# Performance work log

Measured on AMD Instinct MI355X. Metric: run time of the kernel, lower is better.

Reference implementation:

```python
import jax, jax.numpy as jnp
import numpy as np

PAD = -10000.0
B, N, F = 512, 2048, 16
H_PHI, LAT, H_RHO = 128, 128, 128


def _xavier(key, fan_in, fan_out):
    bound = np.sqrt(6.0 / (fan_in + fan_out))
    return jax.random.uniform(key, (fan_in, fan_out), jnp.float32, -bound, bound)


def setup_inputs() -> dict:
    key = jax.random.key(0)
    ks = jax.random.split(key, 12)
    x = jax.random.normal(ks[0], (B, N, F), jnp.float32)
    # ragged set lengths: pad tail rows with -10000.0 (the module's padding sentinel)
    lengths = jax.random.randint(ks[1], (B,), 1, N + 1)
    pad_mask = jnp.arange(N)[None, :] >= lengths[:, None]  # True where padded
    x = jnp.where(pad_mask[:, :, None], PAD, x)
    params = {
        "phi_w0": _xavier(ks[2], F, H_PHI), "phi_b0": jnp.zeros((H_PHI,), jnp.float32),
        "phi_w1": _xavier(ks[3], H_PHI, H_PHI), "phi_b1": jnp.zeros((H_PHI,), jnp.float32),
        "phi_w2": _xavier(ks[4], H_PHI, H_PHI), "phi_b2": jnp.zeros((H_PHI,), jnp.float32),
        "phi_w3": _xavier(ks[5], H_PHI, LAT), "phi_b3": jnp.zeros((LAT,), jnp.float32),
        "rho_w0": _xavier(ks[6], LAT, H_RHO), "rho_b0": jnp.zeros((H_RHO,), jnp.float32),
        "rho_w1": _xavier(ks[7], H_RHO, H_RHO), "rho_b1": jnp.zeros((H_RHO,), jnp.float32),
        "rho_w2": _xavier(ks[8], H_RHO, H_RHO), "rho_b2": jnp.zeros((H_RHO,), jnp.float32),
        "rho_w3": _xavier(ks[9], H_RHO, 1), "rho_b3": jnp.zeros((1,), jnp.float32),
    }
    return {"inputs": x, **params}


def reference(inputs, phi_w0, phi_b0, phi_w1, phi_b1, phi_w2, phi_b2, phi_w3, phi_b3,
              rho_w0, rho_b0, rho_w1, rho_b1, rho_w2, rho_b2, rho_w3, rho_b3):
    b, n, f = inputs.shape
    # valid-prefix mask: sum rows before the FIRST all-(-10000) row (matches torch loop)
    is_pad = jnp.all(inputs == PAD, axis=-1)                       # [B,N]
    first = jnp.where(jnp.any(is_pad, axis=-1), jnp.argmax(is_pad, axis=-1), n)
    mask = (jnp.arange(n)[None, :] < first[:, None]).astype(inputs.dtype)  # [B,N]
    relu = jax.nn.relu
    # phi applied per point
    h = relu(inputs @ phi_w0 + phi_b0)
    h = relu(h @ phi_w1 + phi_b1)
    h = relu(h @ phi_w2 + phi_b2)
    h = relu(h @ phi_w3 + phi_b3)                                  # [B,N,LAT]
    # masked variable-length sum pooling (segment reduce)
    pooled = jnp.einsum('bnd,bn->bd', h, mask)                     # [B,LAT]
    r = relu(pooled @ rho_w0 + rho_b0)
    r = relu(r @ rho_w1 + rho_b1)
    r = relu(r @ rho_w2 + rho_b2)
    cost = (r @ rho_w3 + rho_b3)[:, 0]                             # [B]
    return cost
```

## Files before the change

kernel.cpp:

```cpp
#include <hip/hip_runtime.h>

typedef _Float16 f16;
typedef f16  f16x2  __attribute__((ext_vector_type(2)));
typedef f16  f16x8  __attribute__((ext_vector_type(8)));
typedef __fp16 h16x2 __attribute__((ext_vector_type(2)));
typedef float f32x16 __attribute__((ext_vector_type(16)));

#define B_   512
#define N_   2048
#define PADV -10000.0f

union F16x8 { f16x8 v; f16x2 h2[4]; };

__device__ __forceinline__ f16x2 pkrtz(float a, float b) {
    h16x2 r = __builtin_amdgcn_cvt_pkrtz(a, b);
    return __builtin_bit_cast(f16x2, r);
}

__global__ void prep_kernel(const float* __restrict__ w0, const float* __restrict__ w1,
                            const float* __restrict__ w2, const float* __restrict__ w3,
                            f16* __restrict__ out, float* __restrict__ pooled)
{
    int i = blockIdx.x * 256 + threadIdx.x;
    if (i < 2048) {
        out[i] = (f16)w0[(i & 15) * 128 + (i >> 4)];
    } else if (i < 51200) {
        int j = i - 2048;
        int l = j >> 14, r = j & 16383;
        int o = r >> 7, slot = r & 127;
        int s = slot >> 4, qq = (slot >> 3) & 1, jj = slot & 7;
        int sig = 32 * (s >> 1) + 16 * (s & 1) + 4 * qq + 8 * (jj >> 2) + (jj & 3);
        const float* w = (l == 0) ? w1 : (l == 1) ? w2 : w3;
        out[i] = (f16)w[sig * 128 + o];
    }
    pooled[i] = 0.f;
}

__device__ __forceinline__ int swz(int row, int chunk) {
    return row * 256 + ((chunk ^ (row & 15)) << 4);
}

__device__ __forceinline__ void gl_lds16(const void* g, void* l) {
    __builtin_amdgcn_global_load_lds(
        (const __attribute__((address_space(1))) void*)g,
        (__attribute__((address_space(3))) void*)l, 16, 0, 0);
}

__global__ __launch_bounds__(256, 2) void phi_pool_kernel(
    const float* __restrict__ x,
    const f16*  __restrict__ wtbuf,
    const float* __restrict__ pb0, const float* __restrict__ pb1,
    const float* __restrict__ pb2, const float* __restrict__ pb3,
    float* __restrict__ pooled)
{
    __shared__ f16 wA[16384];
    __shared__ f16 wB[16384];

    const int tid  = threadIdx.x;
    const int lane = tid & 63;
    const int wv   = tid >> 6;
    const int l31  = lane & 31;
    const int q    = lane >> 5;
    const int b    = blockIdx.x & 511;
    const int tile0 = (blockIdx.x >> 9) * 256;

    {
        const float4 f0 = *(const float4*)(x + ((size_t)b * N_ + tile0) * 16);
        if (f0.x == PADV && f0.y == PADV && f0.z == PADV && f0.w == PADV) return;
    }

    const int p0 = tile0 + wv * 64;

    const float* xp = x + ((size_t)b * N_ + (size_t)(p0 + l31)) * 16 + 8 * q;
    float4 a0 = ((const float4*)xp)[0];
    float4 a1 = ((const float4*)xp)[1];
    float4 c0 = ((const float4*)(xp + 512))[0];
    float4 c1 = ((const float4*)(xp + 512))[1];

    f16x8 w0f[4];
    #pragma unroll
    for (int c = 0; c < 4; ++c)
        w0f[c] = *(const f16x8*)(wtbuf + (32 * c + l31) * 16 + 8 * q);

    {
        const f16* wl1 = wtbuf + 2048;
        const f16* wl2 = wtbuf + 2048 + 16384;
        #pragma unroll
        for (int i = 0; i < 8; ++i) {
            const int row   = wv * 32 + i * 4 + (lane >> 4);
            const int chunk = (lane & 15) ^ (row & 15);
            const int loff  = (wv * 32 + i * 4) * 256;
            gl_lds16(wl1 + row * 128 + chunk * 8, (char*)wA + loff);
            gl_lds16(wl2 + row * 128 + chunk * 8, (char*)wB + loff);
        }
    }

    bool vA = (a0.x != PADV) || (a0.y != PADV) || (a0.z != PADV) || (a0.w != PADV) ||
              (a1.x != PADV) || (a1.y != PADV) || (a1.z != PADV) || (a1.w != PADV);
    bool vB = (c0.x != PADV) || (c0.y != PADV) || (c0.z != PADV) || (c0.w != PADV) ||
              (c1.x != PADV) || (c1.y != PADV) || (c1.z != PADV) || (c1.w != PADV);
    unsigned long long blA = __ballot(vA), blB = __ballot(vB);
    const unsigned mA = (unsigned)blA | (unsigned)(blA >> 32);
    const unsigned mB = (unsigned)blB | (unsigned)(blB >> 32);

    F16x8 hf[2][8];
    hf[0][0].h2[0] = pkrtz(a0.x, a0.y);
    hf[0][0].h2[1] = pkrtz(a0.z, a0.w);
    hf[0][0].h2[2] = pkrtz(a1.x, a1.y);
    hf[0][0].h2[3] = pkrtz(a1.z, a1.w);
    hf[1][0].h2[0] = pkrtz(c0.x, c0.y);
    hf[1][0].h2[1] = pkrtz(c0.z, c0.w);
    hf[1][0].h2[2] = pkrtz(c1.x, c1.y);
    hf[1][0].h2[3] = pkrtz(c1.z, c1.w);

    f32x16 acc[2][4];

    #define INIT_ACC_BIAS(pb)                                              \
        {                                                                  \
            _Pragma("unroll")                                              \
            for (int c = 0; c < 4; ++c) {                                  \
                _Pragma("unroll")                                          \
                for (int g = 0; g < 4; ++g) {                              \
                    float4 bb = *(const float4*)((pb) + 32 * c + 8 * g + 4 * q); \
                    const float* bbp = (const float*)&bb;                  \
                    _Pragma("unroll")                                      \
                    for (int e = 0; e < 4; ++e) {                          \
                        acc[0][c][4 * g + e] = bbp[e];                     \
                        acc[1][c][4 * g + e] = bbp[e];                     \
                    }                                                      \
                }                                                          \
            }                                                              \
        }

    #define EPILOGUE()                                                     \
        {                                                                  \
            const f16x2 z2 = {(f16)0.f, (f16)0.f};                         \
            _Pragma("unroll")                                              \
            for (int t = 0; t < 2; ++t) {                                  \
                _Pragma("unroll")                                          \
                for (int s = 0; s < 8; ++s) {                              \
                    const int c = s >> 1, r0 = 8 * (s & 1);                \
                    _Pragma("unroll")                                      \
                    for (int p = 0; p < 4; ++p) {                          \
                        f16x2 m = pkrtz(                                   \
                            acc[t][c][r0 + 2 * p], acc[t][c][r0 + 2 * p + 1]); \
                        hf[t][s].h2[p] = __builtin_elementwise_max(m, z2); \
                    }                                                      \
                }                                                          \
            }                                                              \
        }

    INIT_ACC_BIAS(pb0);
    #pragma unroll
    for (int c = 0; c < 4; ++c) {
        acc[0][c] = __builtin_amdgcn_mfma_f32_32x32x16_f16(w0f[c], hf[0][0].v, acc[0][c], 0, 0, 0);
        acc[1][c] = __builtin_amdgcn_mfma_f32_32x32x16_f16(w0f[c], hf[1][0].v, acc[1][c], 0, 0, 0);
    }
    EPILOGUE();

    __syncthreads();

    INIT_ACC_BIAS(pb1);
    #pragma unroll
    for (int s = 0; s < 8; ++s) {
        f16x8 wf[4];
        #pragma unroll
        for (int c = 0; c < 4; ++c)
            wf[c] = *(const f16x8*)((const char*)wA + swz(32 * c + l31, 2 * s + q));
        #pragma unroll
        for (int c = 0; c < 4; ++c) {
            acc[0][c] = __builtin_amdgcn_mfma_f32_32x32x16_f16(wf[c], hf[0][s].v, acc[0][c], 0, 0, 0);
            acc[1][c] = __builtin_amdgcn_mfma_f32_32x32x16_f16(wf[c], hf[1][s].v, acc[1][c], 0, 0, 0);
        }
    }

    __syncthreads();

    {
        const f16* wl3 = wtbuf + 2048 + 32768;
        #pragma unroll
        for (int i = 0; i < 8; ++i) {
            const int row   = wv * 32 + i * 4 + (lane >> 4);
            const int chunk = (lane & 15) ^ (row & 15);
            const int loff  = (wv * 32 + i * 4) * 256;
            gl_lds16(wl3 + row * 128 + chunk * 8, (char*)wA + loff);
        }
    }

    EPILOGUE();

    INIT_ACC_BIAS(pb2);
    #pragma unroll
    for (int s = 0; s < 8; ++s) {
        f16x8 wf[4];
        #pragma unroll
        for (int c = 0; c < 4; ++c)
            wf[c] = *(const f16x8*)((const char*)wB + swz(32 * c + l31, 2 * s + q));
        #pragma unroll
        for (int c = 0; c < 4; ++c) {
            acc[0][c] = __builtin_amdgcn_mfma_f32_32x32x16_f16(wf[c], hf[0][s].v, acc[0][c], 0, 0, 0);
            acc[1][c] = __builtin_amdgcn_mfma_f32_32x32x16_f16(wf[c], hf[1][s].v, acc[1][c], 0, 0, 0);
        }
    }
    EPILOGUE();

    __syncthreads();

    {
        float bL[4];
        #pragma unroll
        for (int c = 0; c < 4; ++c) bL[c] = pb3[32 * c + l31];
        #pragma unroll
        for (int t = 0; t < 2; ++t)
            #pragma unroll
            for (int c = 0; c < 4; ++c)
                #pragma unroll
                for (int r = 0; r < 16; ++r) acc[t][c][r] = bL[c];
    }
    #pragma unroll
    for (int s = 0; s < 8; ++s) {
        f16x8 wf[4];
        #pragma unroll
        for (int c = 0; c < 4; ++c)
            wf[c] = *(const f16x8*)((const char*)wA + swz(32 * c + l31, 2 * s + q));
        #pragma unroll
        for (int c = 0; c < 4; ++c) {
            acc[0][c] = __builtin_amdgcn_mfma_f32_32x32x16_f16(hf[0][s].v, wf[c], acc[0][c], 0, 0, 0);
            acc[1][c] = __builtin_amdgcn_mfma_f32_32x32x16_f16(hf[1][s].v, wf[c], acc[1][c], 0, 0, 0);
        }
    }

    #pragma unroll
    for (int c = 0; c < 4; ++c) {
        float s0 = 0.f;
        #pragma unroll
        for (int t = 0; t < 2; ++t) {
            const unsigned m = t ? mB : mA;
            #pragma unroll
            for (int r = 0; r < 16; ++r) {
                const int ptl = 4 * q + (r & 3) + 8 * (r >> 2);
                float v = fmaxf(acc[t][c][r], 0.f);
                s0 += ((m >> ptl) & 1u) ? v : 0.f;
            }
        }
        s0 += __shfl_xor(s0, 32);
        if (q == 0) atomicAdd(&pooled[b * 128 + 32 * c + l31], s0);
    }
}

__global__ __launch_bounds__(128) void rho_kernel(
    const float* __restrict__ pooled,
    const float* __restrict__ w0, const float* __restrict__ b0,
    const float* __restrict__ w1, const float* __restrict__ b1,
    const float* __restrict__ w2, const float* __restrict__ b2,
    const float* __restrict__ w3, const float* __restrict__ b3,
    float* __restrict__ out)
{
    __shared__ float buf[2][128];
    __shared__ float red[2];
    const int b = blockIdx.x, t = threadIdx.x;
    buf[0][t] = pooled[b * 128 + t];
    __syncthreads();
    const float* ws3[3] = {w0, w1, w2};
    const float* bs3[3] = {b0, b1, b2};
    int cur = 0;
    #pragma unroll 1
    for (int l = 0; l < 3; ++l) {
        float acc = bs3[l][t];
        const float* w = ws3[l];
        #pragma unroll 8
        for (int k = 0; k < 128; ++k)
            acc = fmaf(buf[cur][k], w[k * 128 + t], acc);
        buf[cur ^ 1][t] = fmaxf(acc, 0.f);
        cur ^= 1;
        __syncthreads();
    }
    float v = buf[cur][t] * w3[t];
    #pragma unroll
    for (int off = 32; off > 0; off >>= 1)
        v += __shfl_down(v, off, 64);
    if ((t & 63) == 0) red[t >> 6] = v;
    __syncthreads();
    if (t == 0) out[b] = red[0] + red[1] + b3[0];
}

extern "C" void kernel_launch(void* const* d_in, const int* in_sizes, int n_in,
                              void* d_out, int out_size, void* d_ws, size_t ws_size,
                              hipStream_t stream)
{
    (void)in_sizes; (void)n_in; (void)out_size; (void)ws_size;
    const float* x      = (const float*)d_in[0];
    const float* phi_w0 = (const float*)d_in[1];
    const float* phi_b0 = (const float*)d_in[2];
    const float* phi_w1 = (const float*)d_in[3];
    const float* phi_b1 = (const float*)d_in[4];
    const float* phi_w2 = (const float*)d_in[5];
    const float* phi_b2 = (const float*)d_in[6];
    const float* phi_w3 = (const float*)d_in[7];
    const float* phi_b3 = (const float*)d_in[8];
    const float* rho_w0 = (const float*)d_in[9];
    const float* rho_b0 = (const float*)d_in[10];
    const float* rho_w1 = (const float*)d_in[11];
    const float* rho_b1 = (const float*)d_in[12];
    const float* rho_w2 = (const float*)d_in[13];
    const float* rho_b2 = (const float*)d_in[14];
    const float* rho_w3 = (const float*)d_in[15];
    const float* rho_b3 = (const float*)d_in[16];

    float* pooled = (float*)d_ws;
    f16*   wtbuf  = (f16*)((char*)d_ws + 262144);

    prep_kernel<<<256, 256, 0, stream>>>(phi_w0, phi_w1, phi_w2, phi_w3, wtbuf, pooled);
    phi_pool_kernel<<<4096, 256, 0, stream>>>(x, wtbuf, phi_b0, phi_b1, phi_b2, phi_b3, pooled);
    rho_kernel<<<B_, 128, 0, stream>>>(pooled, rho_w0, rho_b0, rho_w1, rho_b1,
                                       rho_w2, rho_b2, rho_w3, rho_b3, (float*)d_out);
}
```

Measured before the change: 205.0 us.

## Halve per-block tile and use single LDS weight buffer for higher occupancy

Each block now handles 128 points instead of 256, with one 32-point MFMA tile per wave instead of two. The grid doubles to 8192 blocks and launch bounds rise to 4 blocks per CU. The two 32KB LDS weight buffers become one 32KB buffer that is restaged for each layer, with extra barriers between layers. This is meant to raise occupancy and give finer early exit on padded tiles. The cost is less reuse of the weights pulled from LDS, and weight staging becomes serialized behind the barriers.

```diff
diff --git a/kernel.cpp b/kernel.cpp
--- a/kernel.cpp
+++ b/kernel.cpp
@@ -46,15 +46,14 @@
         (__attribute__((address_space(3))) void*)l, 16, 0, 0);
 }
 
-__global__ __launch_bounds__(256, 2) void phi_pool_kernel(
+__global__ __launch_bounds__(256, 4) void phi_pool_kernel(
     const float* __restrict__ x,
     const f16*  __restrict__ wtbuf,
     const float* __restrict__ pb0, const float* __restrict__ pb1,
     const float* __restrict__ pb2, const float* __restrict__ pb3,
     float* __restrict__ pooled)
 {
-    __shared__ f16 wA[16384];
-    __shared__ f16 wB[16384];
+    __shared__ f16 wS[16384];
 
     const int tid  = threadIdx.x;
     const int lane = tid & 63;
@@ -62,58 +61,49 @@
     const int l31  = lane & 31;
     const int q    = lane >> 5;
     const int b    = blockIdx.x & 511;
-    const int tile0 = (blockIdx.x >> 9) * 256;
+    const int tile0 = (blockIdx.x >> 9) * 128;
 
     {
         const float4 f0 = *(const float4*)(x + ((size_t)b * N_ + tile0) * 16);
         if (f0.x == PADV && f0.y == PADV && f0.z == PADV && f0.w == PADV) return;
     }
 
-    const int p0 = tile0 + wv * 64;
+    const int p0 = tile0 + wv * 32;
 
     const float* xp = x + ((size_t)b * N_ + (size_t)(p0 + l31)) * 16 + 8 * q;
     float4 a0 = ((const float4*)xp)[0];
     float4 a1 = ((const float4*)xp)[1];
-    float4 c0 = ((const float4*)(xp + 512))[0];
-    float4 c1 = ((const float4*)(xp + 512))[1];
 
     f16x8 w0f[4];
     #pragma unroll
     for (int c = 0; c < 4; ++c)
         w0f[c] = *(const f16x8*)(wtbuf + (32 * c + l31) * 16 + 8 * q);
 
-    {
-        const f16* wl1 = wtbuf + 2048;
-        const f16* wl2 = wtbuf + 2048 + 16384;
-        #pragma unroll
-        for (int i = 0; i < 8; ++i) {
-            const int row   = wv * 32 + i * 4 + (lane >> 4);
-            const int chunk = (lane & 15) ^ (row & 15);
-            const int loff  = (wv * 32 + i * 4) * 256;
-            gl_lds16(wl1 + row * 128 + chunk * 8, (char*)wA + loff);
-            gl_lds16(wl2 + row * 128 + chunk * 8, (char*)wB + loff);
-        }
-    }
+#define STAGE(src)                                                      \
+    {                                                                   \
+        _Pragma("unroll")                                               \
+        for (int i = 0; i < 8; ++i) {                                   \
+            const int row   = wv * 32 + i * 4 + (lane >> 4);            \
+            const int chunk = (lane & 15) ^ (row & 15);                 \
+            const int loff  = (wv * 32 + i * 4) * 256;   \
+            gl_lds16((src) + row * 128 + chunk * 8, (char*)wS + loff);  \
+        }                                                               \
+    }
+
+    STAGE(wtbuf + 2048);
 
     bool vA = (a0.x != PADV) || (a0.y != PADV) || (a0.z != PADV) || (a0.w != PADV) ||
               (a1.x != PADV) || (a1.y != PADV) || (a1.z != PADV) || (a1.w != PADV);
-    bool vB = (c0.x != PADV) || (c0.y != PADV) || (c0.z != PADV) || (c0.w != PADV) ||
-              (c1.x != PADV) || (c1.y != PADV) || (c1.z != PADV) || (c1.w != PADV);
-    unsigned long long blA = __ballot(vA), blB = __ballot(vB);
+    unsigned long long blA = __ballot(vA);
     const unsigned mA = (unsigned)blA | (unsigned)(blA >> 32);
-    const unsigned mB = (unsigned)blB | (unsigned)(blB >> 32);
-
-    F16x8 hf[2][8];
-    hf[0][0].h2[0] = pkrtz(a0.x, a0.y);
-    hf[0][0].h2[1] = pkrtz(a0.z, a0.w);
-    hf[0][0].h2[2] = pkrtz(a1.x, a1.y);
-    hf[0][0].h2[3] = pkrtz(a1.z, a1.w);
-    hf[1][0].h2[0] = pkrtz(c0.x, c0.y);
-    hf[1][0].h2[1] = pkrtz(c0.z, c0.w);
-    hf[1][0].h2[2] = pkrtz(c1.x, c1.y);
-    hf[1][0].h2[3] = pkrtz(c1.z, c1.w);
-
-    f32x16 acc[2][4];
+
+    F16x8 hf[8];
+    hf[0].h2[0] = pkrtz(a0.x, a0.y);
+    hf[0].h2[1] = pkrtz(a0.z, a0.w);
+    hf[0].h2[2] = pkrtz(a1.x, a1.y);
+    hf[0].h2[3] = pkrtz(a1.z, a1.w);
+
+    f32x16 acc[4];
 
     #define INIT_ACC_BIAS(pb)                                              \
         {                                                                  \
@@ -124,10 +114,8 @@
                     float4 bb = *(const float4*)((pb) + 32 * c + 8 * g + 4 * q); \
                     const float* bbp = (const float*)&bb;                  \
                     _Pragma("unroll")                                      \
-                    for (int e = 0; e < 4; ++e) {                          \
-                        acc[0][c][4 * g + e] = bbp[e];                     \
-                        acc[1][c][4 * g + e] = bbp[e];                     \
-                    }                                                      \
+                    for (int e = 0; e < 4; ++e)                            \
+                        acc[c][4 * g + e] = bbp[e];                        \
                 }                                                          \
             }                                                              \
         }
@@ -136,112 +124,88 @@
         {                                                                  \
             const f16x2 z2 = {(f16)0.f, (f16)0.f};                         \
             _Pragma("unroll")                                              \
-            for (int t = 0; t < 2; ++t) {                                  \
+            for (int s = 0; s < 8; ++s) {                                  \
+                const int c = s >> 1, r0 = 8 * (s & 1);                    \
                 _Pragma("unroll")                                          \
-                for (int s = 0; s < 8; ++s) {                              \
-                    const int c = s >> 1, r0 = 8 * (s & 1);                \
-                    _Pragma("unroll")                                      \
-                    for (int p = 0; p < 4; ++p) {                          \
-                        f16x2 m = pkrtz(                                   \
-                            acc[t][c][r0 + 2 * p], acc[t][c][r0 + 2 * p + 1]); \
-                        hf[t][s].h2[p] = __builtin_elementwise_max(m, z2); \
-                    }                                                      \
+                for (int p = 0; p < 4; ++p) {                              \
+                    f16x2 m = pkrtz(                                       \
+                        acc[c][r0 + 2 * p], acc[c][r0 + 2 * p + 1]);       \
+                    hf[s].h2[p] = __builtin_elementwise_max(m, z2);        \
                 }                                                          \
             }                                                              \
         }
 
     INIT_ACC_BIAS(pb0);
     #pragma unroll
-    for (int c = 0; c < 4; ++c) {
-        acc[0][c] = __builtin_amdgcn_mfma_f32_32x32x16_f16(w0f[c], hf[0][0].v, acc[0][c], 0, 0, 0);
-        acc[1][c] = __builtin_amdgcn_mfma_f32_32x32x16_f16(w0f[c], hf[1][0].v, acc[1][c], 0, 0, 0);
-    }
+    for (int c = 0; c < 4; ++c)
+        acc[c] = __builtin_amdgcn_mfma_f32_32x32x16_f16(w0f[c], hf[0].v, acc[c], 0, 0, 0);
     EPILOGUE();
-
-    __syncthreads();
-
     INIT_ACC_BIAS(pb1);
+
+    __syncthreads();
+
     #pragma unroll
     for (int s = 0; s < 8; ++s) {
         f16x8 wf[4];
         #pragma unroll
         for (int c = 0; c < 4; ++c)
-            wf[c] = *(const f16x8*)((const char*)wA + swz(32 * c + l31, 2 * s + q));
-        #pragma unroll
-        for (int c = 0; c < 4; ++c) {
-            acc[0][c] = __builtin_amdgcn_mfma_f32_32x32x16_f16(wf[c], hf[0][s].v, acc[0][c], 0, 0, 0);
-            acc[1][c] = __builtin_amdgcn_mfma_f32_32x32x16_f16(wf[c], hf[1][s].v, acc[1][c], 0, 0, 0);
-        }
-    }
-
-    __syncthreads();
-
-    {
-        const f16* wl3 = wtbuf + 2048 + 32768;
-        #pragma unroll
-        for (int i = 0; i < 8; ++i) {
-            const int row   = wv * 32 + i * 4 + (lane >> 4);
-            const int chunk = (lane & 15) ^ (row & 15);
-            const int loff  = (wv * 32 + i * 4) * 256;
-            gl_lds16(wl3 + row * 128 + chunk * 8, (char*)wA + loff);
-        }
-    }
-
+            wf[c] = *(const f16x8*)((const char*)wS + swz(32 * c + l31, 2 * s + q));
+        #pragma unroll
+        for (int c = 0; c < 4; ++c)
+            acc[c] = __builtin_amdgcn_mfma_f32_32x32x16_f16(wf[c], hf[s].v, acc[c], 0, 0, 0);
+    }
+
+    __syncthreads();
+    STAGE(wtbuf + 2048 + 16384);
     EPILOGUE();
-
     INIT_ACC_BIAS(pb2);
+    __syncthreads();
+
     #pragma unroll
     for (int s = 0; s < 8; ++s) {
         f16x8 wf[4];
         #pragma unroll
         for (int c = 0; c < 4; ++c)
-            wf[c] = *(const f16x8*)((const char*)wB + swz(32 * c + l31, 2 * s + q));
-        #pragma unroll
-        for (int c = 0; c < 4; ++c) {
-            acc[0][c] = __builtin_amdgcn_mfma_f32_32x32x16_f16(wf[c], hf[0][s].v, acc[0][c], 0, 0, 0);
-            acc[1][c] = __builtin_amdgcn_mfma_f32_32x32x16_f16(wf[c], hf[1][s].v, acc[1][c], 0, 0, 0);
-        }
-    }
+            wf[c] = *(const f16x8*)((const char*)wS + swz(32 * c + l31, 2 * s + q));
+        #pragma unroll
+        for (int c = 0; c < 4; ++c)
+            acc[c] = __builtin_amdgcn_mfma_f32_32x32x16_f16(wf[c], hf[s].v, acc[c], 0, 0, 0);
+    }
+
+    __syncthreads();
+    STAGE(wtbuf + 2048 + 32768);
     EPILOGUE();
-
-    __syncthreads();
 
     {
         float bL[4];
         #pragma unroll
         for (int c = 0; c < 4; ++c) bL[c] = pb3[32 * c + l31];
         #pragma unroll
-        for (int t = 0; t < 2; ++t)
+        for (int c = 0; c < 4; ++c)
             #pragma unroll
-            for (int c = 0; c < 4; ++c)
-                #pragma unroll
-                for (int r = 0; r < 16; ++r) acc[t][c][r] = bL[c];
-    }
+            for (int r = 0; r < 16; ++r) acc[c][r] = bL[c];
+    }
+    __syncthreads();
+
     #pragma unroll
     for (int s = 0; s < 8; ++s) {
         f16x8 wf[4];
         #pragma unroll
         for (int c = 0; c < 4; ++c)
-            wf[c] = *(const f16x8*)((const char*)wA + swz(32 * c + l31, 2 * s + q));
-        #pragma unroll
-        for (int c = 0; c < 4; ++c) {
-            acc[0][c] = __builtin_amdgcn_mfma_f32_32x32x16_f16(hf[0][s].v, wf[c], acc[0][c], 0, 0, 0);
-            acc[1][c] = __builtin_amdgcn_mfma_f32_32x32x16_f16(hf[1][s].v, wf[c], acc[1][c], 0, 0, 0);
-        }
+            wf[c] = *(const f16x8*)((const char*)wS + swz(32 * c + l31, 2 * s + q));
+        #pragma unroll
+        for (int c = 0; c < 4; ++c)
+            acc[c] = __builtin_amdgcn_mfma_f32_32x32x16_f16(hf[s].v, wf[c], acc[c], 0, 0, 0);
     }
 
     #pragma unroll
     for (int c = 0; c < 4; ++c) {
         float s0 = 0.f;
         #pragma unroll
-        for (int t = 0; t < 2; ++t) {
-            const unsigned m = t ? mB : mA;
-            #pragma unroll
-            for (int r = 0; r < 16; ++r) {
-                const int ptl = 4 * q + (r & 3) + 8 * (r >> 2);
-                float v = fmaxf(acc[t][c][r], 0.f);
-                s0 += ((m >> ptl) & 1u) ? v : 0.f;
-            }
+        for (int r = 0; r < 16; ++r) {
+            const int ptl = 4 * q + (r & 3) + 8 * (r >> 2);
+            float v = fmaxf(acc[c][r], 0.f);
+            s0 += ((mA >> ptl) & 1u) ? v : 0.f;
         }
         s0 += __shfl_xor(s0, 32);
         if (q == 0) atomicAdd(&pooled[b * 128 + 32 * c + l31], s0);
@@ -311,7 +275,7 @@
     f16*   wtbuf  = (f16*)((char*)d_ws + 262144);
 
     prep_kernel<<<256, 256, 0, stream>>>(phi_w0, phi_w1, phi_w2, phi_w3, wtbuf, pooled);
-    phi_pool_kernel<<<4096, 256, 0, stream>>>(x, wtbuf, phi_b0, phi_b1, phi_b2, phi_b3, pooled);
+    phi_pool_kernel<<<8192, 256, 0, stream>>>(x, wtbuf, phi_b0, phi_b1, phi_b2, phi_b3, pooled);
     rho_kernel<<<B_, 128, 0, stream>>>(pooled, rho_w0, rho_b0, rho_w1, rho_b1,
                                        rho_w2, rho_b2, rho_w3, rho_b3, (float*)d_out);
 }
```

Measured after the change: 265.0 us. 1.29x slower.

## Convert phi kernel to persistent blocks with work-stealing and resident layer weights

Applied to the files above, without the earlier changes.

Swaps the 4096-block grid, which reloaded layer weights into LDS for every 256-point tile, for 256 persistent 512-thread blocks. Each block loads all three 128x128 layer weights into 96KB of dynamic LDS once, then its waves pull (tile, batch-group) work items from per-wave atomic counters initialised in the prep kernel. This amortises weight staging and removes the intra-block barriers between layers. In exchange it uses more LDS per block, which lowers occupancy, adds atomic contention on the counters, and handles one 64-point tile per wave iteration rather than a 256-point block.

```diff
diff --git a/kernel.cpp b/kernel.cpp
--- a/kernel.cpp
+++ b/kernel.cpp
@@ -19,7 +19,8 @@
 
 __global__ void prep_kernel(const float* __restrict__ w0, const float* __restrict__ w1,
                             const float* __restrict__ w2, const float* __restrict__ w3,
-                            f16* __restrict__ out, float* __restrict__ pooled)
+                            f16* __restrict__ out, float* __restrict__ pooled,
+                            unsigned* __restrict__ cnt)
 {
     int i = blockIdx.x * 256 + threadIdx.x;
     if (i < 2048) {
@@ -34,6 +35,7 @@
         out[i] = (f16)w[sig * 128 + o];
     }
     pooled[i] = 0.f;
+    if (blockIdx.x == 255 && threadIdx.x < 8) cnt[threadIdx.x] = 256u;
 }
 
 __device__ __forceinline__ int swz(int row, int chunk) {
@@ -46,74 +48,46 @@
         (__attribute__((address_space(3))) void*)l, 16, 0, 0);
 }
 
-__global__ __launch_bounds__(256, 2) void phi_pool_kernel(
+__global__ __launch_bounds__(512, 2) void phi_pool_kernel(
     const float* __restrict__ x,
     const f16*  __restrict__ wtbuf,
     const float* __restrict__ pb0, const float* __restrict__ pb1,
     const float* __restrict__ pb2, const float* __restrict__ pb3,
-    float* __restrict__ pooled)
+    float* __restrict__ pooled, unsigned* __restrict__ cnt)
 {
-    __shared__ f16 wA[16384];
-    __shared__ f16 wB[16384];
+    extern __shared__ char smem[];
+    char* wA = smem;
+    char* wB = smem + 32768;
+    char* wC = smem + 65536;
 
     const int tid  = threadIdx.x;
     const int lane = tid & 63;
     const int wv   = tid >> 6;
     const int l31  = lane & 31;
     const int q    = lane >> 5;
-    const int b    = blockIdx.x & 511;
-    const int tile0 = (blockIdx.x >> 9) * 256;
 
     {
-        const float4 f0 = *(const float4*)(x + ((size_t)b * N_ + tile0) * 16);
-        if (f0.x == PADV && f0.y == PADV && f0.z == PADV && f0.w == PADV) return;
-    }
-
-    const int p0 = tile0 + wv * 64;
-
-    const float* xp = x + ((size_t)b * N_ + (size_t)(p0 + l31)) * 16 + 8 * q;
-    float4 a0 = ((const float4*)xp)[0];
-    float4 a1 = ((const float4*)xp)[1];
-    float4 c0 = ((const float4*)(xp + 512))[0];
-    float4 c1 = ((const float4*)(xp + 512))[1];
+        const f16* wsrc = wtbuf + 2048;
+        #pragma unroll
+        for (int i = 0; i < 4; ++i) {
+            const int row   = wv * 16 + i * 4 + (lane >> 4);
+            const int chunk = (lane & 15) ^ (row & 15);
+            const int loff  = (wv * 16 + i * 4) * 256;
+            gl_lds16(wsrc +         row * 128 + chunk * 8, wA + loff);
+            gl_lds16(wsrc + 16384 + row * 128 + chunk * 8, wB + loff);
+            gl_lds16(wsrc + 32768 + row * 128 + chunk * 8, wC + loff);
+        }
+    }
 
     f16x8 w0f[4];
+    float bL[4];
     #pragma unroll
-    for (int c = 0; c < 4; ++c)
+    for (int c = 0; c < 4; ++c) {
         w0f[c] = *(const f16x8*)(wtbuf + (32 * c + l31) * 16 + 8 * q);
-
-    {
-        const f16* wl1 = wtbuf + 2048;
-        const f16* wl2 = wtbuf + 2048 + 16384;
-        #pragma unroll
-        for (int i = 0; i < 8; ++i) {
-            const int row   = wv * 32 + i * 4 + (lane >> 4);
-            const int chunk = (lane & 15) ^ (row & 15);
-            const int loff  = (wv * 32 + i * 4) * 256;
-            gl_lds16(wl1 + row * 128 + chunk * 8, (char*)wA + loff);
-            gl_lds16(wl2 + row * 128 + chunk * 8, (char*)wB + loff);
-        }
-    }
-
-    bool vA = (a0.x != PADV) || (a0.y != PADV) || (a0.z != PADV) || (a0.w != PADV) ||
-              (a1.x != PADV) || (a1.y != PADV) || (a1.z != PADV) || (a1.w != PADV);
-    bool vB = (c0.x != PADV) || (c0.y != PADV) || (c0.z != PADV) || (c0.w != PADV) ||
-              (c1.x != PADV) || (c1.y != PADV) || (c1.z != PADV) || (c1.w != PADV);
-    unsigned long long blA = __ballot(vA), blB = __ballot(vB);
-    const unsigned mA = (unsigned)blA | (unsigned)(blA >> 32);
-    const unsigned mB = (unsigned)blB | (unsigned)(blB >> 32);
-
-    F16x8 hf[2][8];
-    hf[0][0].h2[0] = pkrtz(a0.x, a0.y);
-    hf[0][0].h2[1] = pkrtz(a0.z, a0.w);
-    hf[0][0].h2[2] = pkrtz(a1.x, a1.y);
-    hf[0][0].h2[3] = pkrtz(a1.z, a1.w);
-    hf[1][0].h2[0] = pkrtz(c0.x, c0.y);
-    hf[1][0].h2[1] = pkrtz(c0.z, c0.w);
-    hf[1][0].h2[2] = pkrtz(c1.x, c1.y);
-    hf[1][0].h2[3] = pkrtz(c1.z, c1.w);
-
-    f32x16 acc[2][4];
+        bL[c]  = pb3[32 * c + l31];
+    }
+
+    __syncthreads();
 
     #define INIT_ACC_BIAS(pb)                                              \
         {                                                                  \
@@ -142,109 +116,133 @@
                     const int c = s >> 1, r0 = 8 * (s & 1);                \
                     _Pragma("unroll")                                      \
                     for (int p = 0; p < 4; ++p) {                          \
-                        f16x2 m = pkrtz(                                   \
+                        f16x2 mm = pkrtz(                                  \
                             acc[t][c][r0 + 2 * p], acc[t][c][r0 + 2 * p + 1]); \
-                        hf[t][s].h2[p] = __builtin_elementwise_max(m, z2); \
+                        hf[t][s].h2[p] = __builtin_elementwise_max(mm, z2); \
                     }                                                      \
                 }                                                          \
             }                                                              \
         }
 
-    INIT_ACC_BIAS(pb0);
-    #pragma unroll
-    for (int c = 0; c < 4; ++c) {
-        acc[0][c] = __builtin_amdgcn_mfma_f32_32x32x16_f16(w0f[c], hf[0][0].v, acc[0][c], 0, 0, 0);
-        acc[1][c] = __builtin_amdgcn_mfma_f32_32x32x16_f16(w0f[c], hf[1][0].v, acc[1][c], 0, 0, 0);
-    }
-    EPILOGUE();
-
-    __syncthreads();
-
-    INIT_ACC_BIAS(pb1);
-    #pragma unroll
-    for (int s = 0; s < 8; ++s) {
-        f16x8 wf[4];
-        #pragma unroll
-        for (int c = 0; c < 4; ++c)
-            wf[c] = *(const f16x8*)((const char*)wA + swz(32 * c + l31, 2 * s + q));
-        #pragma unroll
-        for (int c = 0; c < 4; ++c) {
-            acc[0][c] = __builtin_amdgcn_mfma_f32_32x32x16_f16(wf[c], hf[0][s].v, acc[0][c], 0, 0, 0);
-            acc[1][c] = __builtin_amdgcn_mfma_f32_32x32x16_f16(wf[c], hf[1][s].v, acc[1][c], 0, 0, 0);
+    unsigned m = blockIdx.x;
+    unsigned* cp = cnt + wv;
+
+    #pragma unroll 1
+    for (;;) {
+        const int t64 = (int)(m & 31) << 6;
+        const int db0 = (int)((m >> 5) << 2);
+        #pragma unroll 1
+        for (int k = 0; k < 4; ++k) {
+            const int b = (wv << 6) + db0 + k;
+            const float* xr = x + ((size_t)b * N_ + t64) * 16;
+            const float4 f0 = *(const float4*)xr;
+            if (f0.x == PADV && f0.y == PADV && f0.z == PADV && f0.w == PADV)
+                continue;
+
+            const float* xp = xr + l31 * 16 + 8 * q;
+            float4 a0 = ((const float4*)xp)[0];
+            float4 a1 = ((const float4*)xp)[1];
+            float4 c0 = ((const float4*)(xp + 512))[0];
+            float4 c1 = ((const float4*)(xp + 512))[1];
+
+            bool vA = (a0.x != PADV) || (a0.y != PADV) || (a0.z != PADV) || (a0.w != PADV) ||
+                      (a1.x != PADV) || (a1.y != PADV) || (a1.z != PADV) || (a1.w != PADV);
+            bool vB = (c0.x != PADV) || (c0.y != PADV) || (c0.z != PADV) || (c0.w != PADV) ||
+                      (c1.x != PADV) || (c1.y != PADV) || (c1.z != PADV) || (c1.w != PADV);
+            unsigned long long blA = __ballot(vA), blB = __ballot(vB);
+            const unsigned mskA = (unsigned)blA | (unsigned)(blA >> 32);
+            const unsigned mskB = (unsigned)blB | (unsigned)(blB >> 32);
+
+            F16x8 hf[2][8];
+            hf[0][0].h2[0] = pkrtz(a0.x, a0.y);
+            hf[0][0].h2[1] = pkrtz(a0.z, a0.w);
+            hf[0][0].h2[2] = pkrtz(a1.x, a1.y);
+            hf[0][0].h2[3] = pkrtz(a1.z, a1.w);
+            hf[1][0].h2[0] = pkrtz(c0.x, c0.y);
+            hf[1][0].h2[1] = pkrtz(c0.z, c0.w);
+            hf[1][0].h2[2] = pkrtz(c1.x, c1.y);
+            hf[1][0].h2[3] = pkrtz(c1.z, c1.w);
+
+            f32x16 acc[2][4];
+
+            INIT_ACC_BIAS(pb0);
+            #pragma unroll
+            for (int c = 0; c < 4; ++c) {
+                acc[0][c] = __builtin_amdgcn_mfma_f32_32x32x16_f16(w0f[c], hf[0][0].v, acc[0][c], 0, 0, 0);
+                acc[1][c] = __builtin_amdgcn_mfma_f32_32x32x16_f16(w0f[c], hf[1][0].v, acc[1][c], 0, 0, 0);
+            }
+            EPILOGUE();
+
+            INIT_ACC_BIAS(pb1);
+            #pragma unroll
+            for (int s = 0; s < 8; ++s) {
+                f16x8 wf[4];
+                #pragma unroll
+                for (int c = 0; c < 4; ++c)
+                    wf[c] = *(const f16x8*)(wA + swz(32 * c + l31, 2 * s + q));
+                #pragma unroll
+                for (int c = 0; c < 4; ++c) {
+                    acc[0][c] = __builtin_amdgcn_mfma_f32_32x32x16_f16(wf[c], hf[0][s].v, acc[0][c], 0, 0, 0);
+                    acc[1][c] = __builtin_amdgcn_mfma_f32_32x32x16_f16(wf[c], hf[1][s].v, acc[1][c], 0, 0, 0);
+                }
+            }
+            EPILOGUE();
+
+            INIT_ACC_BIAS(pb2);
+            #pragma unroll
+            for (int s = 0; s < 8; ++s) {
+                f16x8 wf[4];
+                #pragma unroll
+                for (int c = 0; c < 4; ++c)
+                    wf[c] = *(const f16x8*)(wB + swz(32 * c + l31, 2 * s + q));
+                #pragma unroll
+                for (int c = 0; c < 4; ++c) {
+                    acc[0][c] = __builtin_amdgcn_mfma_f32_32x32x16_f16(wf[c], hf[0][s].v, acc[0][c], 0, 0, 0);
+                    acc[1][c] = __builtin_amdgcn_mfma_f32_32x32x16_f16(wf[c], hf[1][s].v, acc[1][c], 0, 0, 0);
+                }
+            }
+            EPILOGUE();
+
+            #pragma unroll
+            for (int t = 0; t < 2; ++t)
+                #pragma unroll
+                for (int c = 0; c < 4; ++c)
+                    #pragma unroll
+                    for (int r = 0; r < 16; ++r) acc[t][c][r] = bL[c];
+            #pragma unroll
+            for (int s = 0; s < 8; ++s) {
+                f16x8 wf[4];
+                #pragma unroll
+                for (int c = 0; c < 4; ++c)
+                    wf[c] = *(const f16x8*)(wC + swz(32 * c + l31, 2 * s + q));
+                #pragma unroll
+                for (int c = 0; c < 4; ++c) {
+                    acc[0][c] = __builtin_amdgcn_mfma_f32_32x32x16_f16(hf[0][s].v, wf[c], acc[0][c], 0, 0, 0);
+                    acc[1][c] = __builtin_amdgcn_mfma_f32_32x32x16_f16(hf[1][s].v, wf[c], acc[1][c], 0, 0, 0);
+                }
+            }
+
+            #pragma unroll
+            for (int c = 0; c < 4; ++c) {
+                float s0 = 0.f;
+                #pragma unroll
+                for (int t = 0; t < 2; ++t) {
+                    const unsigned msk = t ? mskB : mskA;
+                    #pragma unroll
+                    for (int r = 0; r < 16; ++r) {
+                        const int ptl = 4 * q + (r & 3) + 8 * (r >> 2);
+                        float v = fmaxf(acc[t][c][r], 0.f);
+                        s0 += ((msk >> ptl) & 1u) ? v : 0.f;
+                    }
+                }
+                s0 += __shfl_xor(s0, 32);
+                if (q == 0) atomicAdd(&pooled[b * 128 + 32 * c + l31], s0);
+            }
         }
-    }
-
-    __syncthreads();
-
-    {
-        const f16* wl3 = wtbuf + 2048 + 32768;
-        #pragma unroll
-        for (int i = 0; i < 8; ++i) {
-            const int row   = wv * 32 + i * 4 + (lane >> 4);
-            const int chunk = (lane & 15) ^ (row & 15);
-            const int loff  = (wv * 32 + i * 4) * 256;
-            gl_lds16(wl3 + row * 128 + chunk * 8, (char*)wA + loff);
-        }
-    }
-
-    EPILOGUE();
-
-    INIT_ACC_BIAS(pb2);
-    #pragma unroll
-    for (int s = 0; s < 8; ++s) {
-        f16x8 wf[4];
-        #pragma unroll
-        for (int c = 0; c < 4; ++c)
-            wf[c] = *(const f16x8*)((const char*)wB + swz(32 * c + l31, 2 * s + q));
-        #pragma unroll
-        for (int c = 0; c < 4; ++c) {
-            acc[0][c] = __builtin_amdgcn_mfma_f32_32x32x16_f16(wf[c], hf[0][s].v, acc[0][c], 0, 0, 0);
-            acc[1][c] = __builtin_amdgcn_mfma_f32_32x32x16_f16(wf[c], hf[1][s].v, acc[1][c], 0, 0, 0);
-        }
-    }
-    EPILOGUE();
-
-    __syncthreads();
-
-    {
-        float bL[4];
-        #pragma unroll
-        for (int c = 0; c < 4; ++c) bL[c] = pb3[32 * c + l31];
-        #pragma unroll
-        for (int t = 0; t < 2; ++t)
-            #pragma unroll
-            for (int c = 0; c < 4; ++c)
-                #pragma unroll
-                for (int r = 0; r < 16; ++r) acc[t][c][r] = bL[c];
-    }
-    #pragma unroll
-    for (int s = 0; s < 8; ++s) {
-        f16x8 wf[4];
-        #pragma unroll
-        for (int c = 0; c < 4; ++c)
-            wf[c] = *(const f16x8*)((const char*)wA + swz(32 * c + l31, 2 * s + q));
-        #pragma unroll
-        for (int c = 0; c < 4; ++c) {
-            acc[0][c] = __builtin_amdgcn_mfma_f32_32x32x16_f16(hf[0][s].v, wf[c], acc[0][c], 0, 0, 0);
-            acc[1][c] = __builtin_amdgcn_mfma_f32_32x32x16_f16(hf[1][s].v, wf[c], acc[1][c], 0, 0, 0);
-        }
-    }
-
-    #pragma unroll
-    for (int c = 0; c < 4; ++c) {
-        float s0 = 0.f;
-        #pragma unroll
-        for (int t = 0; t < 2; ++t) {
-            const unsigned m = t ? mB : mA;
-            #pragma unroll
-            for (int r = 0; r < 16; ++r) {
-                const int ptl = 4 * q + (r & 3) + 8 * (r >> 2);
-                float v = fmaxf(acc[t][c][r], 0.f);
-                s0 += ((m >> ptl) & 1u) ? v : 0.f;
-            }
-        }
-        s0 += __shfl_xor(s0, 32);
-        if (q == 0) atomicAdd(&pooled[b * 128 + 32 * c + l31], s0);
+        unsigned mn = 0;
+        if (lane == 0) mn = atomicAdd(cp, 1u);
+        m = (unsigned)__builtin_amdgcn_readfirstlane((int)mn);
+        if (m >= 512u) break;
     }
 }
 
@@ -307,11 +305,20 @@
     const float* rho_w3 = (const float*)d_in[15];
     const float* rho_b3 = (const float*)d_in[16];
 
-    float* pooled = (float*)d_ws;
-    f16*   wtbuf  = (f16*)((char*)d_ws + 262144);
-
-    prep_kernel<<<256, 256, 0, stream>>>(phi_w0, phi_w1, phi_w2, phi_w3, wtbuf, pooled);
-    phi_pool_kernel<<<4096, 256, 0, stream>>>(x, wtbuf, phi_b0, phi_b1, phi_b2, phi_b3, pooled);
+    float*    pooled = (float*)d_ws;
+    f16*      wtbuf  = (f16*)((char*)d_ws + 262144);
+    unsigned* cnt    = (unsigned*)((char*)d_ws + 364544);
+
+    static int smem_set = 0;
+    if (!smem_set) {
+        hipFuncSetAttribute((const void*)phi_pool_kernel,
+                            hipFuncAttributeMaxDynamicSharedMemorySize, 98304);
+        smem_set = 1;
+    }
+
+    prep_kernel<<<256, 256, 0, stream>>>(phi_w0, phi_w1, phi_w2, phi_w3, wtbuf, pooled, cnt);
+    phi_pool_kernel<<<256, 512, 98304, stream>>>(x, wtbuf, phi_b0, phi_b1, phi_b2, phi_b3,
+                                                 pooled, cnt);
     rho_kernel<<<B_, 128, 0, stream>>>(pooled, rho_w0, rho_b0, rho_w1, rho_b1,
                                        rho_w2, rho_b2, rho_w3, rho_b3, (float*)d_out);
 }
```

Result: slower. 239.3 us (+16.7%).
